# Kernel optimization log

Hardware: AMD Instinct MI355X
Metric: run time of the kernel (lower is better)

## Reference

```python
import jax, jax.numpy as jnp
import numpy as np

N = 8192      # number of nodes
D = 256       # embedding dim
K = 32        # k_degree
EPS = 1e-6


def setup_inputs() -> dict:
    key = jax.random.key(0)
    k1, k2 = jax.random.split(key)
    x = jax.random.normal(k1, (N, D), dtype=jnp.float32)
    q = jax.random.uniform(k2, (N, N), dtype=jnp.float32)  # gumbel uniform noise
    temperature = jnp.array([0.001], dtype=jnp.float32)    # learned nn.Parameter
    return {"x": x, "q": q, "temperature": temperature}


def reference(x, q, temperature):
    # torch: dist_mat = sum(x - x.unsqueeze(1), dim=-1) ** 2
    # dist_mat[i, j] = (sum_f x[j,f] - sum_f x[i,f])^2 = (s[j] - s[i])^2
    s = jnp.sum(x, axis=-1)                      # [N]
    dist_mat = (s[None, :] - s[:, None]) ** 2    # [N, N]
    probs = jnp.exp(-temperature[0] * dist_mat) + EPS

    # Gumbel-perturbed logits, top-k per column via argsort along axis 0
    g = jnp.log(probs + EPS) - jnp.log(-jnp.log(q + EPS))  # [N, N]
    child_nodes = jnp.argsort(g, axis=0)[-K:].reshape(-1)   # [K*N]
    parent_nodes = jnp.tile(jnp.arange(N, dtype=child_nodes.dtype), K)  # [K*N]

    # symmetric scatter of adjacency mask
    mask = jnp.zeros((N, N), dtype=x.dtype)
    mask = mask.at[child_nodes, parent_nodes].set(1.0)
    mask = mask.at[parent_nodes, child_nodes].set(1.0)

    edge_index = jnp.stack([child_nodes, parent_nodes])      # [2, K*N]
    edge_weights = jnp.ones((edge_index.shape[1],), dtype=x.dtype)
    return edge_index, edge_weights, probs, mask, dist_mat
```

## Files before the change

kernel.cpp:

```cpp
#include <hip/hip_runtime.h>
#include <stdint.h>

typedef unsigned long long ull;
typedef float __attribute__((ext_vector_type(4))) floatx4;
#define NN 8192
#define KK 32

__device__ __forceinline__ ull make_key(float g, uint32_t idx) {
    uint32_t b = __float_as_uint(g);
    uint32_t k = b ^ (0x80000000u | (uint32_t)((int32_t)b >> 31));
    return ((ull)k << 32) | idx;
}

__device__ __forceinline__ void cas_both(ull &a, ull &b) {
    ull x = a, y = b;
    bool g = x < y;
    a = g ? y : x;
    b = g ? x : y;
}

__device__ __forceinline__ void sort16_desc(ull (&c)[16]) {
#pragma unroll
    for (int k = 2; k <= 16; k <<= 1) {
#pragma unroll
        for (int j = k >> 1; j > 0; j >>= 1) {
#pragma unroll
            for (int i = 0; i < 16; ++i) {
                int l = i ^ j;
                if (l > i) {
                    if ((i & k) == 0) cas_both(c[i], c[l]);
                    else              cas_both(c[l], c[i]);
                }
            }
        }
    }
}

__device__ __forceinline__ void bmerge32_desc(ull (&c)[32]) {
#pragma unroll
    for (int j = 16; j > 0; j >>= 1) {
#pragma unroll
        for (int i = 0; i < 32; ++i) {
            if ((i & j) == 0) cas_both(c[i], c[i ^ j]);
        }
    }
}

__device__ __forceinline__ void merge_into32(ull (&acc)[32], const ull (&ch)[32]) {
#pragma unroll
    for (int k = 0; k < 32; ++k) {
        ull a = acc[31 - k], b = ch[k];
        acc[31 - k] = a >= b ? a : b;
    }
    bmerge32_desc(acc);
}

__device__ __forceinline__ void load_list32(const ull* __restrict__ src, int list,
                                            int j, ull (&ch)[32]) {
#pragma unroll
    for (int k = 0; k < 32; ++k)
        ch[k] = src[((size_t)list * 32 + k) * NN + j];
}

__global__ __launch_bounds__(256) void k_rowsum(const float* __restrict__ x,
                                                float* __restrict__ s) {
    int row  = blockIdx.x * 4 + (threadIdx.x >> 6);
    int lane = threadIdx.x & 63;
    float4 v = reinterpret_cast<const float4*>(x)[(size_t)row * 64 + lane];
    float sum = (v.x + v.y) + (v.z + v.w);
#pragma unroll
    for (int off = 1; off < 64; off <<= 1) sum += __shfl_xor(sum, off, 64);
    if (lane == 0) s[row] = sum;
}

__global__ __launch_bounds__(256, 4) void k_fused(const float* __restrict__ q,
                                                  const float* __restrict__ s,
                                                  const float* __restrict__ tptr,
                                                  float* __restrict__ dist_out,
                                                  float* __restrict__ probs_out,
                                                  float* __restrict__ mask,
                                                  ull* __restrict__ cand,
                                                  int segr, int nthreads) {
    const uint32_t j = blockIdx.x * 256 + threadIdx.x;
    const uint32_t gtid =
        (blockIdx.y * (NN / 256) + blockIdx.x) * 256 + threadIdx.x;
    const float sj = s[j];
    const float temp = tptr[0];

    ull top[32];
#pragma unroll
    for (int k = 0; k < 32; ++k) top[k] = 0;

    const uint32_t i0 = (uint32_t)blockIdx.y * (uint32_t)segr;
    for (uint32_t r = 0; r < (uint32_t)segr; r += 16) {
        const uint32_t it = r >> 4;
        const uint32_t ib = i0 + r;
        const uint32_t off0 = ib * NN + j;

        ull ch[16];
        {
            float qv[8];
#pragma unroll
            for (uint32_t u = 0; u < 8; ++u) qv[u] = q[off0 + u * NN];
#pragma unroll
            for (uint32_t u = 0; u < 8; ++u) {
                float diff = sj - s[ib + u];
                float d = diff * diff;
                float pr = expf(-(temp * d)) + 1e-6f;
                uint32_t off = off0 + u * NN;
                dist_out[off]  = d;
                probs_out[off] = pr;
                float a = logf(pr + 1e-6f);
                float b = logf(-logf(qv[u] + 1e-6f));
                ch[u] = make_key(a - b, ib + u);
            }
        }
        {
            float qv[8];
#pragma unroll
            for (uint32_t u = 0; u < 8; ++u) qv[u] = q[off0 + (8 + u) * NN];
#pragma unroll
            for (uint32_t u = 0; u < 8; ++u) {
                float diff = sj - s[ib + 8 + u];
                float d = diff * diff;
                float pr = expf(-(temp * d)) + 1e-6f;
                uint32_t off = off0 + (8 + u) * NN;
                dist_out[off]  = d;
                probs_out[off] = pr;
                float a = logf(pr + 1e-6f);
                float b = logf(-logf(qv[u] + 1e-6f));
                ch[8 + u] = make_key(a - b, ib + 8 + u);
            }
        }
        {
            floatx4* mask4 = (floatx4*)mask;
            const floatx4 z4 = {0.f, 0.f, 0.f, 0.f};
#pragma unroll
            for (uint32_t u = 0; u < 4; ++u)
                mask4[(it * 4 + u) * (uint32_t)nthreads + gtid] = z4;
        }

        sort16_desc(ch);
#pragma unroll
        for (int u = 0; u < 16; ++u) {
            ull a = top[16 + u], b = ch[15 - u];
            top[16 + u] = a >= b ? a : b;
        }
        bmerge32_desc(top);
    }
    const uint32_t base = (uint32_t)blockIdx.y * (KK * NN) + j;
#pragma unroll
    for (uint32_t k = 0; k < KK; ++k) cand[base + k * NN] = top[k];
}

__global__ __launch_bounds__(256) void k_merge1(const ull* __restrict__ src,
                                                ull* __restrict__ dst,
                                                int lists_per_grp) {
    int gid = blockIdx.x * 256 + threadIdx.x;
    int j   = gid & (NN - 1);
    int grp = gid >> 13;
    ull acc[32];
    load_list32(src, grp * lists_per_grp, j, acc);
    for (int l = 1; l < lists_per_grp; ++l) {
        ull ch[32];
        load_list32(src, grp * lists_per_grp + l, j, ch);
        merge_into32(acc, ch);
    }
    const size_t base = (size_t)grp * KK * NN + j;
#pragma unroll
    for (int k = 0; k < KK; ++k) dst[base + (size_t)k * NN] = acc[k];
}

__global__ __launch_bounds__(64) void k_final(const ull* __restrict__ src,
                                              float* __restrict__ out,
                                              float* __restrict__ mask) {
    const int j = blockIdx.x * 64 + threadIdx.x;
    ull acc[32];
    load_list32(src, 0, j, acc);
#pragma unroll
    for (int l = 1; l < 4; ++l) {
        ull ch[32];
        load_list32(src, l, j, ch);
        merge_into32(acc, ch);
    }
    const size_t KN = (size_t)KK * NN;
    float* child  = out;
    float* parent = out + KN;
    float* wts    = out + 2 * KN;
#pragma unroll
    for (int k = 0; k < KK; ++k) {
        uint32_t c = (uint32_t)acc[KK - 1 - k];
        child [(size_t)k * NN + j] = (float)c;
        parent[(size_t)k * NN + j] = (float)j;
        wts   [(size_t)k * NN + j] = 1.0f;
        mask[(size_t)c * NN + j] = 1.0f;
        mask[(size_t)j * NN + c] = 1.0f;
    }
}

extern "C" void kernel_launch(void* const* d_in, const int* in_sizes, int n_in,
                              void* d_out, int out_size, void* d_ws, size_t ws_size,
                              hipStream_t stream) {
    const float* x    = (const float*)d_in[0];
    const float* q    = (const float*)d_in[1];
    const float* tptr = (const float*)d_in[2];
    float* out = (float*)d_out;

    const size_t KN = (size_t)KK * NN;
    float* probs_out = out + 3 * KN;
    float* mask_out  = out + 3 * KN + (size_t)NN * NN;
    float* dist_out  = out + 3 * KN + 2 * (size_t)NN * NN;

    const size_t cand1_bytes = (size_t)NN * 4 * KK * 8;
    int nseg = 32;
    if (ws_size < 65536 + (size_t)NN * 32 * KK * 8 + cand1_bytes) nseg = 16;
    const int segr = NN / nseg;
    const int nthreads = (NN / 256) * nseg * 256;
    float* s = (float*)d_ws;
    ull* cand0 = (ull*)((char*)d_ws + 65536);
    ull* cand1 = cand0 + (size_t)NN * nseg * KK;

    k_rowsum<<<NN / 4, 256, 0, stream>>>(x, s);
    k_fused<<<dim3(NN / 256, nseg), 256, 0, stream>>>(
        q, s, tptr, dist_out, probs_out, mask_out, cand0, segr, nthreads);
    k_merge1<<<(NN * 4) / 256, 256, 0, stream>>>(cand0, cand1, nseg / 4);
    k_final<<<NN / 64, 64, 0, stream>>>(cand1, out, mask_out);
}
```

Baseline: 367.5 us.

## Stage q loads and dist/probs stores through LDS with 16-byte nontemporal accesses

Each wavefront now loads its 16x64 tile of q as 16-byte vectors into per-wave LDS, computes from LDS, and writes dist and probs back through LDS as 16-byte nontemporal stores. The mask zeroing stores also become nontemporal. The aim is wider memory transactions and less cache pollution on this bandwidth-bound streaming kernel. In exchange the kernel uses 32 KB of LDS per block and adds LDS round-trips, which may limit occupancy. It relies on wave-synchronous execution without barriers, since each wave only touches its own LDS region.

```diff
diff --git a/kernel.cpp b/kernel.cpp
--- a/kernel.cpp
+++ b/kernel.cpp
@@ -81,11 +81,19 @@
                                                   float* __restrict__ mask,
                                                   ull* __restrict__ cand,
                                                   int segr, int nthreads) {
-    const uint32_t j = blockIdx.x * 256 + threadIdx.x;
+    __shared__ float ldsA[4][16][64];
+    __shared__ float ldsB[4][16][64];
+
+    const uint32_t tid = threadIdx.x;
+    const uint32_t w = tid >> 6, l = tid & 63;
+    const uint32_t j = blockIdx.x * 256 + tid;
+    const uint32_t colbase = blockIdx.x * 256 + w * 64;
     const uint32_t gtid =
-        (blockIdx.y * (NN / 256) + blockIdx.x) * 256 + threadIdx.x;
+        (blockIdx.y * (NN / 256) + blockIdx.x) * 256 + tid;
     const float sj = s[j];
     const float temp = tptr[0];
+    float* A = &ldsA[w][0][0];
+    float* B = &ldsB[w][0][0];
 
     ull top[32];
 #pragma unroll
@@ -95,49 +103,50 @@
     for (uint32_t r = 0; r < (uint32_t)segr; r += 16) {
         const uint32_t it = r >> 4;
         const uint32_t ib = i0 + r;
-        const uint32_t off0 = ib * NN + j;
-
-        ull ch[16];
-        {
-            float qv[8];
-#pragma unroll
-            for (uint32_t u = 0; u < 8; ++u) qv[u] = q[off0 + u * NN];
-#pragma unroll
-            for (uint32_t u = 0; u < 8; ++u) {
-                float diff = sj - s[ib + u];
-                float d = diff * diff;
-                float pr = expf(-(temp * d)) + 1e-6f;
-                uint32_t off = off0 + u * NN;
-                dist_out[off]  = d;
-                probs_out[off] = pr;
-                float a = logf(pr + 1e-6f);
-                float b = logf(-logf(qv[u] + 1e-6f));
-                ch[u] = make_key(a - b, ib + u);
-            }
-        }
-        {
-            float qv[8];
-#pragma unroll
-            for (uint32_t u = 0; u < 8; ++u) qv[u] = q[off0 + (8 + u) * NN];
-#pragma unroll
-            for (uint32_t u = 0; u < 8; ++u) {
-                float diff = sj - s[ib + 8 + u];
-                float d = diff * diff;
-                float pr = expf(-(temp * d)) + 1e-6f;
-                uint32_t off = off0 + (8 + u) * NN;
-                dist_out[off]  = d;
-                probs_out[off] = pr;
-                float a = logf(pr + 1e-6f);
-                float b = logf(-logf(qv[u] + 1e-6f));
-                ch[8 + u] = make_key(a - b, ib + 8 + u);
-            }
+
+#pragma unroll
+        for (uint32_t k = 0; k < 4; ++k) {
+            uint32_t f  = k * 64 + l;
+            uint32_t rr = f >> 4, c4 = f & 15;
+            floatx4 v = __builtin_nontemporal_load(
+                reinterpret_cast<const floatx4*>(
+                    q + (ib + rr) * NN + colbase + c4 * 4));
+            *reinterpret_cast<floatx4*>(&A[f * 4]) = v;
         }
         {
             floatx4* mask4 = (floatx4*)mask;
             const floatx4 z4 = {0.f, 0.f, 0.f, 0.f};
 #pragma unroll
             for (uint32_t u = 0; u < 4; ++u)
-                mask4[(it * 4 + u) * (uint32_t)nthreads + gtid] = z4;
+                __builtin_nontemporal_store(
+                    z4, &mask4[(it * 4 + u) * (uint32_t)nthreads + gtid]);
+        }
+
+        ull ch[16];
+#pragma unroll
+        for (uint32_t u = 0; u < 16; ++u) {
+            float qv = A[u * 64 + l];
+            float diff = sj - s[ib + u];
+            float d = diff * diff;
+            float pr = expf(-(temp * d)) + 1e-6f;
+            B[u * 64 + l] = d;
+            float a = logf(pr + 1e-6f);
+            float bb = logf(-logf(qv + 1e-6f));
+            ch[u] = make_key(a - bb, ib + u);
+            A[u * 64 + l] = pr;
+        }
+
+#pragma unroll
+        for (uint32_t k = 0; k < 4; ++k) {
+            uint32_t f  = k * 64 + l;
+            uint32_t rr = f >> 4, c4 = f & 15;
+            uint32_t goff = (ib + rr) * NN + colbase + c4 * 4;
+            floatx4 dv = *reinterpret_cast<floatx4*>(&B[f * 4]);
+            __builtin_nontemporal_store(
+                dv, reinterpret_cast<floatx4*>(dist_out + goff));
+            floatx4 pv = *reinterpret_cast<floatx4*>(&A[f * 4]);
+            __builtin_nontemporal_store(
+                pv, reinterpret_cast<floatx4*>(probs_out + goff));
         }
 
         sort16_desc(ch);
```

New measurement: 399.3 us. 8.6% more time.
